# Performance work log

Hardware: AMD Instinct MI355X
Metric: run time of the kernel (lower is better)

## Reference

```python
import jax, jax.numpy as jnp
import numpy as np

N_EMBD = 2048
N_HEAD = 16
KV_GROUP = 4
HEAD_DIM = N_EMBD // N_HEAD          # 128
N_KV = N_HEAD // KV_GROUP            # 4
KV_DIM = N_KV * HEAD_DIM             # 512
B, T = 2, 2048
ROPE_THETA = 1000000.0


def setup_inputs() -> dict:
    key = jax.random.key(0)
    k0, k1, k2 = jax.random.split(key, 3)
    x = jax.random.normal(k0, (B, T, N_EMBD), dtype=jnp.float32)
    # weights stored (in, out); matches torch Linear math up to a transpose of random init
    W_attn = jax.random.normal(k1, (N_EMBD, N_EMBD + 2 * KV_DIM), dtype=jnp.float32) * 0.02
    b_attn = jnp.zeros((N_EMBD + 2 * KV_DIM,), dtype=jnp.float32)
    W_proj = jax.random.normal(k2, (N_EMBD, N_EMBD), dtype=jnp.float32) * 0.02
    # realistic RoPE frequencies (Qwen-style theta)
    inv_freq = 1.0 / (ROPE_THETA ** (np.arange(0, HEAD_DIM, 2, dtype=np.float64) / HEAD_DIM))
    ang = np.outer(np.arange(T, dtype=np.float64), inv_freq)  # (T, HEAD_DIM//2)
    freqs_cos = jnp.asarray(np.cos(ang), dtype=jnp.float32)
    freqs_sin = jnp.asarray(np.sin(ang), dtype=jnp.float32)
    return {"x": x, "W_attn": W_attn, "b_attn": b_attn, "W_proj": W_proj,
            "freqs_cos": freqs_cos, "freqs_sin": freqs_sin}


def _rope_expand(x, cos, sin, kv_group):
    # x: (B, T, n_kv, hd); complex rotate interleaved pairs, then expand to n_kv*kv_group heads
    Bx, Tx, nh, hd = x.shape
    xf = x.astype(jnp.float32).reshape(Bx, Tx, nh, hd // 2, 2)
    a, b = xf[..., 0], xf[..., 1]
    c = cos[None, :, None, :]  # (1, T, 1, hd//2)
    s = sin[None, :, None, :]
    yr = a * c - b * s
    yi = a * s + b * c
    y = jnp.stack([yr, yi], axis=-1).reshape(Bx, Tx, nh, hd)
    y = jnp.broadcast_to(y[:, :, :, None, :], (Bx, Tx, nh, kv_group, hd))
    return y.reshape(Bx, Tx, nh * kv_group, hd).astype(x.dtype)


def reference(x, W_attn, b_attn, W_proj, freqs_cos, freqs_sin):
    Bx, Tx, E = x.shape
    hd = 2 * freqs_cos.shape[-1]
    n_q = E // hd
    kv_dim = (W_attn.shape[1] - E) // 2
    n_kv = kv_dim // hd
    g = n_q // n_kv

    qkv = x @ W_attn + b_attn  # (B, T, E + 2*kv_dim)
    q = qkv[..., :E].reshape(Bx, Tx, n_q, hd).transpose(0, 2, 1, 3)          # bhtd
    k = qkv[..., E:E + kv_dim].reshape(Bx, Tx, n_kv, hd)
    v = qkv[..., E + kv_dim:].reshape(Bx, Tx, n_kv, hd)
    # faithful to source: RoPE on K AND V (not Q), then GQA expand
    k = _rope_expand(k, freqs_cos, freqs_sin, g).transpose(0, 2, 1, 3)       # bhtd
    v = _rope_expand(v, freqs_cos, freqs_sin, g).transpose(0, 2, 1, 3)       # bhtd

    scale = 1.0 / jnp.sqrt(jnp.asarray(hd, dtype=x.dtype))
    scores = jnp.einsum('bhqd,bhkd->bhqk', q, k) * scale                     # (B, H, T, T)
    causal = jnp.tril(jnp.ones((Tx, Tx), dtype=bool))
    scores = jnp.where(causal, scores, jnp.asarray(-jnp.inf, scores.dtype))
    attn = jax.nn.softmax(scores, axis=-1)
    y = jnp.einsum('bhqk,bhkd->bhqd', attn, v)
    y = y.transpose(0, 2, 1, 3).reshape(Bx, Tx, E)
    return y @ W_proj  # c_proj, no bias
```

## Files before the change

kernel.cpp:

```cpp
#include <hip/hip_runtime.h>
#include <cstdint>
#include <cstddef>

#define T_SEQ 2048
#define B_SZ  2
#define EMB   2048
#define NH    16
#define NKV   4
#define HD    128
#define KVD   512
#define QKVN  3072
#define MROWS (B_SZ*T_SEQ)

typedef __bf16 bf16x8 __attribute__((ext_vector_type(8)));
typedef float  f32x4  __attribute__((ext_vector_type(4)));
typedef short  s16x8  __attribute__((ext_vector_type(8)));
typedef unsigned short u16;

__device__ __forceinline__ u16 f2b(float f) {
  uint32_t u = __builtin_bit_cast(uint32_t, f);
  u += 0x7fffu + ((u >> 16) & 1u);
  return (u16)(u >> 16);
}
__device__ __forceinline__ float b2f(u16 h) {
  return __builtin_bit_cast(float, (uint32_t)h << 16);
}
__device__ __forceinline__ bf16x8 ld_bf8(const u16* p) {
  return __builtin_bit_cast(bf16x8, *(const s16x8*)p);
}
__device__ __forceinline__ void glds16(const void* g, void* l) {
  __builtin_amdgcn_global_load_lds((const __attribute__((address_space(1))) void*)g,
                                   (__attribute__((address_space(3))) void*)l, 16, 0, 0);
}
template<int N> __device__ __forceinline__ void waitv() {
  if constexpr (N == 0) asm volatile("s_waitcnt vmcnt(0)" ::: "memory");
  else if constexpr (N == 2) asm volatile("s_waitcnt vmcnt(2)" ::: "memory");
  else if constexpr (N == 3) asm volatile("s_waitcnt vmcnt(3)" ::: "memory");
  __builtin_amdgcn_sched_barrier(0);
}

__global__ void cvt_x_kernel(const float4* __restrict__ x, ushort4* __restrict__ xb, int n4) {
  int i = blockIdx.x*blockDim.x + threadIdx.x;
  if (i >= n4) return;
  float4 v = x[i];
  ushort4 o;
  o.x = f2b(v.x); o.y = f2b(v.y); o.z = f2b(v.z); o.w = f2b(v.w);
  xb[i] = o;
}

__global__ void transpose_w_kernel(const float* __restrict__ in, u16* __restrict__ out,
                                   int R, int C) {
  __shared__ float tile[32][33];
  int c0 = blockIdx.x*32, r0 = blockIdx.y*32;
  int tx = threadIdx.x, ty = threadIdx.y;
#pragma unroll
  for (int i = 0; i < 32; i += 8)
    tile[ty+i][tx] = in[(size_t)(r0+ty+i)*C + c0+tx];
  __syncthreads();
#pragma unroll
  for (int i = 0; i < 32; i += 8)
    out[(size_t)(c0+ty+i)*R + r0+tx] = f2b(tile[tx][ty+i]);
}

template<int BN, int WGN, int MF, int NF, int NF1, int SB, int SB1, int VMC, bool BF16_OUT>
__global__ __launch_bounds__(512, 2) void gemm_kernel(const u16* __restrict__ A,
        const u16* __restrict__ Bt, const float* __restrict__ bias,
        void* __restrict__ Cout, int M, int N, int K) {
  constexpr int MF2 = MF/2;
  __shared__ u16 As[2][256*64];
  __shared__ u16 Bs[2][BN*64];
  const int tid = threadIdx.x;
  const int w = tid >> 6, lane = tid & 63;
  const int quad = lane >> 4, lc = lane & 15;
  const int wrow = w / WGN, wcol = w % WGN;
  const int gx = gridDim.x;
  const int lin = blockIdx.y*gx + blockIdx.x;
  const int swz = (lin & 7)*32 + (lin >> 3);
  const int m0 = (swz / gx)*256, n0 = (swz % gx)*BN;

  f32x4 acc[MF][NF] = {};
  bf16x8 af[MF2][2], bfv[NF][2];

  int xoff[2];
#pragma unroll
  for (int ks = 0; ks < 2; ++ks) xoff[ks] = ((ks*4 + quad) ^ (lc & 7))*8;
  const int arow0 = (wrow*MF*16 + lc)*64;
  const int brow0 = (wcol*NF*16 + lc)*64;

  const int srb  = tid >> 3;
  const int spos = (tid & 7) ^ (srb & 7);
  const u16* sAp = A  + (size_t)(m0 + srb)*K + spos*8;
  const u16* sBp = Bt + (size_t)(n0 + srb)*K + spos*8;

#define STAGE_A(bf_, t_, h_) do { \
    glds16(sAp + (size_t)((h_)*2  )*64*K + (size_t)(t_)*64, &As[bf_][((h_)*2  )*4096 + w*512]); \
    glds16(sAp + (size_t)((h_)*2+1)*64*K + (size_t)(t_)*64, &As[bf_][((h_)*2+1)*4096 + w*512]); \
  } while (0)
#define STAGE_B(bf_, t_, p_) do { \
    _Pragma("unroll") for (int r = (p_) ? SB1 : 0; r < ((p_) ? SB : SB1); ++r) \
      glds16(sBp + (size_t)r*64*K + (size_t)(t_)*64, &Bs[bf_][r*4096 + w*512]); \
  } while (0)
#define LDAH(S_, h_) do { _Pragma("unroll") for (int i = 0; i < MF2; ++i) { \
    af[i][0] = ld_bf8((S_) + arow0 + ((h_)*MF2 + i)*1024 + xoff[0]); \
    af[i][1] = ld_bf8((S_) + arow0 + ((h_)*MF2 + i)*1024 + xoff[1]); } } while (0)
#define LDBG(S_, g_) do { _Pragma("unroll") for (int j = (g_) ? NF1 : 0; j < ((g_) ? NF : NF1); ++j) { \
    bfv[j][0] = ld_bf8((S_) + brow0 + j*1024 + xoff[0]); \
    bfv[j][1] = ld_bf8((S_) + brow0 + j*1024 + xoff[1]); } } while (0)
#define CL(h_, g_) do { _Pragma("unroll") for (int ks = 0; ks < 2; ++ks) \
    _Pragma("unroll") for (int i = 0; i < MF2; ++i) \
    _Pragma("unroll") for (int j = (g_) ? NF1 : 0; j < ((g_) ? NF : NF1); ++j) \
      acc[(h_)*MF2+i][j] = __builtin_amdgcn_mfma_f32_16x16x32_bf16( \
          af[i][ks], bfv[j][ks], acc[(h_)*MF2+i][j], 0, 0, 0); } while (0)
#define BARX()  __builtin_amdgcn_s_barrier()
#define SCHB()  __builtin_amdgcn_sched_barrier(0)
#define MFMAPH(h_, g_) do { BARX(); \
    asm volatile("s_waitcnt lgkmcnt(0)" ::: "memory"); SCHB(); \
    __builtin_amdgcn_s_setprio(1); CL(h_, g_); __builtin_amdgcn_s_setprio(0); \
  } while (0)

  const int NT = K >> 6;
  STAGE_B(0, 0, 0); STAGE_B(0, 0, 1);
  STAGE_A(0, 0, 0); STAGE_A(0, 0, 1);
  STAGE_B(1, 1, 0); STAGE_B(1, 1, 1);
  waitv<VMC>();
  BARX(); SCHB();

  for (int t0 = 0; t0 < NT-2; t0 += 2) {
    const u16 *a0 = As[0], *b0 = Bs[0], *a1 = As[1], *b1 = Bs[1];
    LDAH(a0, 0); LDBG(b0, 0); STAGE_A(1, t0+1, 0);
    MFMAPH(0, 0); BARX();
    LDBG(b0, 1); STAGE_A(1, t0+1, 1);
    MFMAPH(0, 1); BARX();
    LDAH(a0, 1); STAGE_B(0, t0+2, 0);
    MFMAPH(1, 0); BARX();
    STAGE_B(0, t0+2, 1);
    MFMAPH(1, 1);
    waitv<VMC>();
    BARX(); SCHB();
    LDAH(a1, 0); LDBG(b1, 0); STAGE_A(0, t0+2, 0);
    MFMAPH(0, 0); BARX();
    LDBG(b1, 1); STAGE_A(0, t0+2, 1);
    MFMAPH(0, 1); BARX();
    LDAH(a1, 1); STAGE_B(1, t0+3, 0);
    MFMAPH(1, 0); BARX();
    STAGE_B(1, t0+3, 1);
    MFMAPH(1, 1);
    waitv<VMC>();
    BARX(); SCHB();
  }
  {
    const u16 *a0 = As[0], *b0 = Bs[0], *a1 = As[1], *b1 = Bs[1];
    LDAH(a0, 0); LDBG(b0, 0); STAGE_A(1, NT-1, 0);
    MFMAPH(0, 0); BARX();
    LDBG(b0, 1); STAGE_A(1, NT-1, 1);
    MFMAPH(0, 1); BARX();
    LDAH(a0, 1);
    MFMAPH(1, 0); BARX();
    MFMAPH(1, 1);
    waitv<0>();
    BARX(); SCHB();
    LDAH(a1, 0); LDBG(b1, 0);
    MFMAPH(0, 0); BARX();
    LDBG(b1, 1);
    MFMAPH(0, 1); BARX();
    LDAH(a1, 1);
    MFMAPH(1, 0); BARX();
    MFMAPH(1, 1);
  }

#undef STAGE_A
#undef STAGE_B
#undef LDAH
#undef LDBG
#undef CL
#undef BARX
#undef SCHB
#undef MFMAPH

#pragma unroll
  for (int j = 0; j < NF; ++j) {
    int col = n0 + wcol*NF*16 + j*16 + lc;
    float bv = BF16_OUT ? bias[col] : 0.0f;
#pragma unroll
    for (int i = 0; i < MF; ++i) {
      int rowb = m0 + wrow*MF*16 + i*16 + quad*4;
#pragma unroll
      for (int r = 0; r < 4; ++r) {
        float v = acc[i][j][r] + bv;
        if (BF16_OUT) ((u16*)Cout)[(size_t)(rowb+r)*N + col] = f2b(v);
        else          ((float*)Cout)[(size_t)(rowb+r)*N + col] = v;
      }
    }
  }
}

__global__ void rope_kernel(const u16* __restrict__ qkv, const float* __restrict__ fc,
                            const float* __restrict__ fs, u16* __restrict__ kout,
                            u16* __restrict__ vout) {
  int tid = threadIdx.x;
  int row = blockIdx.x;
  int i = tid & 63, kv = tid >> 6;
  int t = row & (T_SEQ-1);
  const u16* p = qkv + (size_t)row*QKVN + EMB + kv*HD + 2*i;
  float ka = b2f(p[0]),   kb = b2f(p[1]);
  float va = b2f(p[KVD]), vb = b2f(p[KVD+1]);
  float c = fc[t*64+i], s = fs[t*64+i];
  size_t ob = (size_t)row*KVD + kv*HD + 2*i;
  kout[ob]   = f2b(ka*c - kb*s);
  kout[ob+1] = f2b(ka*s + kb*c);
  vout[ob]   = f2b(va*c - vb*s);
  vout[ob+1] = f2b(va*s + vb*c);
}

__global__ void transpose_v_kernel(const u16* __restrict__ vb, u16* __restrict__ vtb) {
  __shared__ u16 tile[32][33];
  int bkv = blockIdx.z;
  int b = bkv >> 2, kv = bkv & 3;
  int d0 = blockIdx.y*32, t0 = blockIdx.x*32;
  int tx = threadIdx.x, ty = threadIdx.y;
#pragma unroll
  for (int i = 0; i < 32; i += 8)
    tile[ty+i][tx] = vb[(size_t)(b*T_SEQ + t0+ty+i)*KVD + kv*HD + d0 + tx];
  __syncthreads();
#pragma unroll
  for (int i = 0; i < 32; i += 8)
    vtb[(size_t)(bkv*HD + d0+ty+i)*T_SEQ + t0 + tx] = tile[tx][ty+i];
}

__global__ __launch_bounds__(256, 3) void flash_kernel(const u16* __restrict__ qkv,
    const u16* __restrict__ kb, const u16* __restrict__ vtb, u16* __restrict__ yb) {
  constexpr int PP = 72;
  __shared__ u16 Ks[64*128];
  __shared__ u16 Vs[128*64];
  __shared__ u16 Ps[4][16*PP];
  const int tid = threadIdx.x;
  const int w = tid >> 6, lane = tid & 63;
  const int quad = lane >> 4, lc = lane & 15;
  const int bkv = blockIdx.x & 7;
  const int r_  = blockIdx.x >> 3;
  const int b = bkv >> 2, kv = bkv & 3;
  const int h = kv*4 + w;
  const int qbase = (127 - r_)*16;

  bf16x8 qf[4];
  {
    const u16* qp = qkv + (size_t)(b*T_SEQ + qbase + lc)*QKVN + h*HD + quad*8;
#pragma unroll
    for (int ks = 0; ks < 4; ++ks) qf[ks] = ld_bf8(qp + ks*32);
  }

  f32x4 o[8] = {};
  float rs[4] = {0.f, 0.f, 0.f, 0.f};
  const u16* kbase = kb  + (size_t)b*T_SEQ*KVD + kv*HD;
  const u16* vbase = vtb + (size_t)bkv*HD*T_SEQ;
  const int nk = qbase + 16;
  const float cs = 0.08838834764831845f * 1.4426950408889634f;
  u16* pw = Ps[w];

  int koff[4], voff[2];
#pragma unroll
  for (int ks = 0; ks < 4; ++ks) koff[ks] = lc*128 + (((ks*4 + quad) ^ lc)*8);
#pragma unroll
  for (int ks = 0; ks < 2; ++ks) voff[ks] = lc*64 + (((ks*4 + quad) ^ (lc & 7))*8);

  for (int k0 = 0; k0 < nk; k0 += 64) {
    __syncthreads();
#pragma unroll
    for (int rr = 0; rr < 4; ++rr) {
      int krow = (rr*4 + w)*4 + (lane >> 4);
      int ccg  = (lane & 15) ^ (krow & 15);
      glds16(kbase + (size_t)(k0 + krow)*KVD + ccg*8, Ks + (size_t)(rr*4 + w)*512);
    }
#pragma unroll
    for (int rr = 0; rr < 4; ++rr) {
      int vrow = (rr*4 + w)*8 + (lane >> 3);
      int ccg  = (lane & 7) ^ (vrow & 7);
      glds16(vbase + (size_t)vrow*T_SEQ + k0 + ccg*8, Vs + (size_t)(rr*4 + w)*512);
    }
    __syncthreads();

    f32x4 sc[4] = {};
#pragma unroll
    for (int nt = 0; nt < 4; ++nt)
#pragma unroll
      for (int ks = 0; ks < 4; ++ks) {
        bf16x8 kf = ld_bf8(Ks + nt*16*128 + koff[ks]);
        sc[nt] = __builtin_amdgcn_mfma_f32_16x16x32_bf16(qf[ks], kf, sc[nt], 0, 0, 0);
      }

    if (k0 + 63 > qbase) {
#pragma unroll
      for (int nt = 0; nt < 4; ++nt) {
        int key = k0 + nt*16 + lc;
        int qrow = qbase + quad*4;
#pragma unroll
        for (int r = 0; r < 4; ++r) {
          float p = (key <= qrow + r) ? exp2f(sc[nt][r]*cs) : 0.0f;
          rs[r] += p;
          pw[(quad*4 + r)*PP + nt*16 + lc] = f2b(p);
        }
      }
    } else {
#pragma unroll
      for (int nt = 0; nt < 4; ++nt)
#pragma unroll
        for (int r = 0; r < 4; ++r) {
          float p = exp2f(sc[nt][r]*cs);
          rs[r] += p;
          pw[(quad*4 + r)*PP + nt*16 + lc] = f2b(p);
        }
    }

    bf16x8 pa[2];
#pragma unroll
    for (int ks = 0; ks < 2; ++ks)
      pa[ks] = ld_bf8(pw + lc*PP + ks*32 + quad*8);

#pragma unroll
    for (int j = 0; j < 8; ++j)
#pragma unroll
      for (int ks = 0; ks < 2; ++ks) {
        bf16x8 vf = ld_bf8(Vs + j*16*64 + voff[ks]);
        o[j] = __builtin_amdgcn_mfma_f32_16x16x32_bf16(pa[ks], vf, o[j], 0, 0, 0);
      }
  }

#pragma unroll
  for (int r = 0; r < 4; ++r) {
    float v = rs[r];
#pragma unroll
    for (int off2 = 8; off2 >= 1; off2 >>= 1)
      v += __shfl_xor(v, off2);
    float inv = 1.0f / v;
    size_t orow = (size_t)(b*T_SEQ + qbase + quad*4 + r)*EMB + h*HD;
#pragma unroll
    for (int j = 0; j < 8; ++j)
      yb[orow + j*16 + lc] = f2b(o[j][r]*inv);
  }
}

extern "C" void kernel_launch(void* const* d_in, const int* in_sizes, int n_in,
                              void* d_out, int out_size, void* d_ws, size_t ws_size,
                              hipStream_t stream) {
  const float* x      = (const float*)d_in[0];
  const float* W_attn = (const float*)d_in[1];
  const float* b_attn = (const float*)d_in[2];
  const float* W_proj = (const float*)d_in[3];
  const float* fc     = (const float*)d_in[4];
  const float* fs     = (const float*)d_in[5];

  u16* ws   = (u16*)d_ws;
  u16* xb   = ws;
  u16* WaT  = xb   + (size_t)MROWS*EMB;
  u16* qkv  = WaT  + (size_t)QKVN*EMB;
  u16* kbuf = qkv  + (size_t)MROWS*QKVN;
  u16* vb   = kbuf + (size_t)MROWS*KVD;
  u16* vtb  = vb   + (size_t)MROWS*KVD;
  u16* WpT  = WaT;
  u16* yb   = xb;
  float* out = (float*)d_out;

  cvt_x_kernel<<<(MROWS*EMB/4 + 255)/256, 256, 0, stream>>>(
      (const float4*)x, (ushort4*)xb, MROWS*EMB/4);
  transpose_w_kernel<<<dim3(QKVN/32, EMB/32), dim3(32, 8), 0, stream>>>(
      W_attn, WaT, EMB, QKVN);
  gemm_kernel<192, 4, 8, 3, 2, 3, 2, 3, true>
      <<<dim3(QKVN/192, MROWS/256), 512, 0, stream>>>(
      xb, WaT, b_attn, qkv, MROWS, QKVN, EMB);
  rope_kernel<<<MROWS, 256, 0, stream>>>(qkv, fc, fs, kbuf, vb);
  transpose_v_kernel<<<dim3(T_SEQ/32, HD/32, B_SZ*NKV), dim3(32, 8), 0, stream>>>(vb, vtb);
  transpose_w_kernel<<<dim3(EMB/32, EMB/32), dim3(32, 8), 0, stream>>>(
      W_proj, WpT, EMB, EMB);
  flash_kernel<<<dim3(B_SZ*NKV*(T_SEQ/16)), 256, 0, stream>>>(qkv, kbuf, vtb, yb);
  gemm_kernel<128, 2, 4, 4, 2, 2, 1, 2, false>
      <<<dim3(EMB/128, MROWS/256), 512, 0, stream>>>(
      yb, WpT, nullptr, out, MROWS, EMB, EMB);
}
```

Baseline: 285.3 us.

## Double-buffer K/V tiles in flash kernel with async prefetch and setprio

Double-buffers the K and V shared-memory tiles so the global-to-LDS load of the next key block is issued before computing the current one. This cuts the iteration to one barrier instead of two. It also raises wave priority around the MFMA loops and uses the raw exp2 builtin. Shared memory per block doubles, so the occupancy hint drops from 3 to 2 blocks per CU, which risks less latency hiding between blocks.

```diff
diff --git a/kernel.cpp b/kernel.cpp
--- a/kernel.cpp
+++ b/kernel.cpp
@@ -227,11 +227,11 @@
     vtb[(size_t)(bkv*HD + d0+ty+i)*T_SEQ + t0 + tx] = tile[tx][ty+i];
 }
 
-__global__ __launch_bounds__(256, 3) void flash_kernel(const u16* __restrict__ qkv,
+__global__ __launch_bounds__(256, 2) void flash_kernel(const u16* __restrict__ qkv,
     const u16* __restrict__ kb, const u16* __restrict__ vtb, u16* __restrict__ yb) {
   constexpr int PP = 72;
-  __shared__ u16 Ks[64*128];
-  __shared__ u16 Vs[128*64];
+  __shared__ u16 Ks[2][64*128];
+  __shared__ u16 Vs[2][128*64];
   __shared__ u16 Ps[4][16*PP];
   const int tid = threadIdx.x;
   const int w = tid >> 6, lane = tid & 63;
@@ -254,60 +254,83 @@
   const u16* kbase = kb  + (size_t)b*T_SEQ*KVD + kv*HD;
   const u16* vbase = vtb + (size_t)bkv*HD*T_SEQ;
   const int nk = qbase + 16;
+  const int nt = (nk + 63) >> 6;
   const float cs = 0.08838834764831845f * 1.4426950408889634f;
   u16* pw = Ps[w];
 
+  const u16* kptr[4];
+  const u16* vptr[4];
+#pragma unroll
+  for (int rr = 0; rr < 4; ++rr) {
+    int krow = (rr*4 + w)*4 + (lane >> 4);
+    int kcc  = (lane & 15) ^ (krow & 15);
+    kptr[rr] = kbase + (size_t)krow*KVD + kcc*8;
+    int vrow = (rr*4 + w)*8 + (lane >> 3);
+    int vcc  = (lane & 7) ^ (vrow & 7);
+    vptr[rr] = vbase + (size_t)vrow*T_SEQ + vcc*8;
+  }
+
   int koff[4], voff[2];
 #pragma unroll
   for (int ks = 0; ks < 4; ++ks) koff[ks] = lc*128 + (((ks*4 + quad) ^ lc)*8);
 #pragma unroll
   for (int ks = 0; ks < 2; ++ks) voff[ks] = lc*64 + (((ks*4 + quad) ^ (lc & 7))*8);
 
-  for (int k0 = 0; k0 < nk; k0 += 64) {
-    __syncthreads();
-#pragma unroll
-    for (int rr = 0; rr < 4; ++rr) {
-      int krow = (rr*4 + w)*4 + (lane >> 4);
-      int ccg  = (lane & 15) ^ (krow & 15);
-      glds16(kbase + (size_t)(k0 + krow)*KVD + ccg*8, Ks + (size_t)(rr*4 + w)*512);
+#pragma unroll
+  for (int rr = 0; rr < 4; ++rr) glds16(kptr[rr], &Ks[0][(rr*4 + w)*512]);
+#pragma unroll
+  for (int rr = 0; rr < 4; ++rr) glds16(vptr[rr], &Vs[0][(rr*4 + w)*512]);
+  asm volatile("s_waitcnt vmcnt(0)" ::: "memory");
+  __builtin_amdgcn_sched_barrier(0);
+  __builtin_amdgcn_s_barrier();
+  __builtin_amdgcn_sched_barrier(0);
+
+  for (int t = 0; t < nt; ++t) {
+    const int cur = t & 1;
+    if (t + 1 < nt) {
+#pragma unroll
+      for (int rr = 0; rr < 4; ++rr)
+        glds16(kptr[rr] + (size_t)(t+1)*64*KVD, &Ks[cur^1][(rr*4 + w)*512]);
+#pragma unroll
+      for (int rr = 0; rr < 4; ++rr)
+        glds16(vptr[rr] + (size_t)(t+1)*64,     &Vs[cur^1][(rr*4 + w)*512]);
     }
-#pragma unroll
-    for (int rr = 0; rr < 4; ++rr) {
-      int vrow = (rr*4 + w)*8 + (lane >> 3);
-      int ccg  = (lane & 7) ^ (vrow & 7);
-      glds16(vbase + (size_t)vrow*T_SEQ + k0 + ccg*8, Vs + (size_t)(rr*4 + w)*512);
-    }
-    __syncthreads();
+    const u16* ksb = Ks[cur];
+    const u16* vsb = Vs[cur];
+    const int k0 = t*64;
 
     f32x4 sc[4] = {};
-#pragma unroll
-    for (int nt = 0; nt < 4; ++nt)
+    __builtin_amdgcn_s_setprio(1);
+#pragma unroll
+    for (int nt2 = 0; nt2 < 4; ++nt2)
 #pragma unroll
       for (int ks = 0; ks < 4; ++ks) {
-        bf16x8 kf = ld_bf8(Ks + nt*16*128 + koff[ks]);
-        sc[nt] = __builtin_amdgcn_mfma_f32_16x16x32_bf16(qf[ks], kf, sc[nt], 0, 0, 0);
+        bf16x8 kf = ld_bf8(ksb + nt2*16*128 + koff[ks]);
+        sc[nt2] = __builtin_amdgcn_mfma_f32_16x16x32_bf16(qf[ks], kf, sc[nt2], 0, 0, 0);
       }
+    __builtin_amdgcn_s_setprio(0);
 
     if (k0 + 63 > qbase) {
 #pragma unroll
-      for (int nt = 0; nt < 4; ++nt) {
-        int key = k0 + nt*16 + lc;
+      for (int nt2 = 0; nt2 < 4; ++nt2) {
+        int key = k0 + nt2*16 + lc;
         int qrow = qbase + quad*4;
 #pragma unroll
         for (int r = 0; r < 4; ++r) {
-          float p = (key <= qrow + r) ? exp2f(sc[nt][r]*cs) : 0.0f;
+          float e = __builtin_amdgcn_exp2f(sc[nt2][r]*cs);
+          float p = (key <= qrow + r) ? e : 0.0f;
           rs[r] += p;
-          pw[(quad*4 + r)*PP + nt*16 + lc] = f2b(p);
+          pw[(quad*4 + r)*PP + nt2*16 + lc] = f2b(p);
         }
       }
     } else {
 #pragma unroll
-      for (int nt = 0; nt < 4; ++nt)
+      for (int nt2 = 0; nt2 < 4; ++nt2)
 #pragma unroll
         for (int r = 0; r < 4; ++r) {
-          float p = exp2f(sc[nt][r]*cs);
+          float p = __builtin_amdgcn_exp2f(sc[nt2][r]*cs);
           rs[r] += p;
-          pw[(quad*4 + r)*PP + nt*16 + lc] = f2b(p);
+          pw[(quad*4 + r)*PP + nt2*16 + lc] = f2b(p);
         }
     }
 
@@ -316,13 +339,20 @@
     for (int ks = 0; ks < 2; ++ks)
       pa[ks] = ld_bf8(pw + lc*PP + ks*32 + quad*8);
 
+    __builtin_amdgcn_s_setprio(1);
 #pragma unroll
     for (int j = 0; j < 8; ++j)
 #pragma unroll
       for (int ks = 0; ks < 2; ++ks) {
-        bf16x8 vf = ld_bf8(Vs + j*16*64 + voff[ks]);
+        bf16x8 vf = ld_bf8(vsb + j*16*64 + voff[ks]);
         o[j] = __builtin_amdgcn_mfma_f32_16x16x32_bf16(pa[ks], vf, o[j], 0, 0, 0);
       }
+    __builtin_amdgcn_s_setprio(0);
+
+    asm volatile("s_waitcnt vmcnt(0)" ::: "memory");
+    __builtin_amdgcn_sched_barrier(0);
+    __builtin_amdgcn_s_barrier();
+    __builtin_amdgcn_sched_barrier(0);
   }
 
 #pragma unroll
```

After: 281.4 us. No clear change (-1.4%).
